# Performance work log

Hardware: AMD Instinct MI355X
Metric: run time of the kernel (lower is better)

## Reference

```python
import jax, jax.numpy as jnp
import numpy as np

DT = 0.1
EM_DX_DUMMY = 100.0  # dummy_value_set['em_delta_x']
EM_DV_DUMMY = 0.0    # dummy_value_set['em_delta_v']
ALPHA = 0.3          # keras LeakyReLU default
B, T, F = 32768, 50, 11
PROJ, U = 64, 128
MC = 3
IN_DIM = PROJ + U + 6 + MC  # 201


def setup_inputs() -> dict:
    key = jax.random.key(0)
    ks = jax.random.split(key, 16)
    def rn(k, shape, scale=0.05):
        return jax.random.normal(k, shape, dtype=jnp.float32) * scale
    return {
        'proj_latent': rn(ks[0], (B, PROJ), 1.0),
        'enc_h': rn(ks[1], (B, U), 1.0),
        'idm_s': jax.random.uniform(ks[2], (B, T, F), dtype=jnp.float32),
        'merger_cs': rn(ks[3], (B, T, MC), 1.0),
        'scaler_mean': rn(ks[4], (6,), 1.0),
        'scaler_var': jax.random.uniform(ks[5], (6,), dtype=jnp.float32) + 0.5,
        'W_lstm': rn(ks[6], (IN_DIM, 4 * U)),
        'U_lstm': rn(ks[7], (U, 4 * U)),
        'b_lstm': jnp.zeros((4 * U,), jnp.float32),
        'W1': rn(ks[8], (U, U)), 'b1': jnp.zeros((U,), jnp.float32),
        'W2': rn(ks[9], (U, U)), 'b2': jnp.zeros((U,), jnp.float32),
        'W3': rn(ks[10], (U, U)), 'b3': jnp.zeros((U,), jnp.float32),
        'Wa': rn(ks[11], (U, 1)), 'ba': jnp.zeros((1,), jnp.float32),
    }


def _lrelu(v):
    return jnp.where(v > 0, v, ALPHA * v)


def reference(proj_latent, enc_h, idm_s, merger_cs, scaler_mean, scaler_var,
              W_lstm, U_lstm, b_lstm, W1, b1, W2, b2, W3, b3, Wa, ba):
    b = idm_s.shape[0]
    u = W1.shape[0]
    inv_std = 1.0 / jnp.sqrt(scaler_var)

    def step(carry, xs):
        h, c, ego_v, ego_x, disp, prev_act = carry
        s, mc, t = xs  # s: [b,F], mc: [b,MC]
        first = (t == 0)
        f_veh_v = s[:, 1:2]
        m_veh_v = s[:, 2:3]
        f_glob_x = s[:, 4:5]
        m_glob_x = s[:, 5:6]
        m_exists = s[:, -1:]
        # physics update (skipped at step 0 where state is read from idm_s)
        new_v = jnp.where(first, s[:, 0:1], ego_v + prev_act * DT)
        delta = new_v * DT + 0.5 * prev_act * DT * DT
        new_x = jnp.where(first, s[:, 3:4], ego_x + delta)
        new_d = jnp.where(first, jnp.zeros_like(disp), disp + delta)
        ef_dx = f_glob_x - new_x
        em_dx = (m_glob_x - new_x) * m_exists + (1.0 - m_exists) * EM_DX_DUMMY
        ef_dv = new_v - f_veh_v
        em_dv = (new_v - m_veh_v) * m_exists + (1.0 - m_exists) * EM_DV_DUMMY
        env = jnp.concatenate([new_v, f_veh_v, ef_dv, ef_dx, em_dv, em_dx], axis=-1)
        env = (env - scaler_mean) * inv_std
        inp = jnp.concatenate([proj_latent, enc_h, env, mc], axis=-1)  # [b, 201]
        # keras LSTM cell: gate order i, f, g(candidate), o
        z = inp @ W_lstm + h @ U_lstm + b_lstm
        i = jax.nn.sigmoid(z[:, :u])
        f = jax.nn.sigmoid(z[:, u:2 * u])
        g = jnp.tanh(z[:, 2 * u:3 * u])
        o = jax.nn.sigmoid(z[:, 3 * u:])
        c2 = f * c + i * g
        h2 = o * jnp.tanh(c2)
        x1 = _lrelu(h2 @ W1 + b1)
        x2 = _lrelu(x1 @ W2 + b2)
        x3 = _lrelu(x2 @ W3 + b3)
        act = x3 @ Wa + ba  # [b, 1]
        return (h2, c2, new_v, new_x, new_d, act), (new_d, act)

    z1 = jnp.zeros((b, u), jnp.float32)
    one = jnp.zeros((b, 1), jnp.float32)
    carry0 = (z1, z1, one, one, one, one)
    xs = (jnp.swapaxes(idm_s, 0, 1), jnp.swapaxes(merger_cs, 0, 1),
          jnp.arange(idm_s.shape[1]))
    _, (disp_seq, act_seq) = jax.lax.scan(step, carry0, xs)
    # [T,b,1] -> [b,T,1]
    return jnp.swapaxes(disp_seq, 0, 1), jnp.swapaxes(act_seq, 0, 1)
```

## Files before the change

kernel.cpp:

```cpp
#include <hip/hip_runtime.h>

typedef unsigned short ushort_t;
typedef unsigned int uint_t;
typedef __bf16 v8bf __attribute__((ext_vector_type(8)));
typedef float v4f __attribute__((ext_vector_type(4)));

#define DTC 0.1f
#define NB 32768
#define NT 50

union U8 { v8bf v; ushort_t s[8]; };

__device__ __forceinline__ ushort_t f2bf(float f) {
  uint_t u = __float_as_uint(f);
  u += 0x7fffu + ((u >> 16) & 1u);
  return (ushort_t)(u >> 16);
}
__device__ __forceinline__ float bf2f(ushort_t s) {
  return __uint_as_float(((uint_t)s) << 16);
}
__device__ __forceinline__ float sigm(float x) {
  return __builtin_amdgcn_rcpf(1.f + __expf(-x));
}
__device__ __forceinline__ float tanhf_(float x) {
  return 1.f - 2.f * __builtin_amdgcn_rcpf(1.f + __expf(2.f * x));
}

__device__ __forceinline__ v8bf opaque(v8bf x) {
  union { v8bf v; uint_t u[4]; } t; t.v = x;
  asm volatile("" : "+v"(t.u[0]), "+v"(t.u[1]), "+v"(t.u[2]), "+v"(t.u[3]));
  return t.v;
}


__global__ __launch_bounds__(512) __attribute__((amdgpu_waves_per_eu(2, 2)))
void fsim_kernel(
    const float* __restrict__ proj, const float* __restrict__ ench,
    const float* __restrict__ idm,  const float* __restrict__ mcs,
    const float* __restrict__ smean,const float* __restrict__ svar,
    const float* __restrict__ Wl,   const float* __restrict__ Ul,
    const float* __restrict__ bl,   const float* __restrict__ W1,
    const float* __restrict__ b1,   const float* __restrict__ W2,
    const float* __restrict__ b2,   const float* __restrict__ W3,
    const float* __restrict__ b3,   const float* __restrict__ Wa,
    const float* __restrict__ ba,   float* __restrict__ out) {
  __shared__ __align__(16) short sh[81184];
  short* pe   = sh;
  short* hA   = sh;
  short* hB   = sh + 8704;
  short* xa_s = sh + 17408;
  short* ex_s = sh + 26112;
  float* sdf  = (float*)(sh + 28672);
  float* carr = (float*)(sh + 31232);
  float* wa_s = (float*)(sh + 31744);
  float* nrm  = (float*)(sh + 32000);
  short* u_lds= sh + 32032;

  const int tid  = threadIdx.x;
  const int wg   = blockIdx.x;
  const int w    = tid >> 6;
  const int l    = tid & 63;
  const int quad = l >> 4;
  const int c16  = l & 15;
  const int colz = w * 16 + c16;

  float* out_disp = out;
  float* out_act  = out + (size_t)NB * NT;

  const int eA = tid / 10, fA = tid - eA * 10;
  const float* pfpA; int pstA;
  if (fA < 7) { pfpA = idm + (size_t)(wg * 64 + eA) * 550 + ((fA == 6) ? 10 : fA); pstA = 11; }
  else        { pfpA = mcs + (size_t)(wg * 64 + eA) * 150 + (fA - 7);              pstA = 3;  }
  const int iB = tid + 512;
  const int eB = iB / 10, fB = iB - eB * 10;
  const float* pfpB; int pstB;
  if (fB < 7) { pfpB = idm + (size_t)(wg * 64 + eB) * 550 + ((fB == 6) ? 10 : fB); pstB = 11; }
  else        { pfpB = mcs + (size_t)(wg * 64 + eB) * 150 + (fB - 7);              pstB = 3;  }
  float pfA = pfpA[0];
  float pfB = (tid < 128) ? pfpB[0] : 0.f;

#pragma unroll
  for (int kc = 0; kc < 3; ++kc) {
#pragma unroll
    for (int g = 0; g < 4; ++g) {
      U8 u;
#pragma unroll
      for (int j = 0; j < 8; ++j)
        u.s[j] = f2bf(Ul[(kc * 32 + quad * 8 + j) * 512 + g * 128 + colz]);
      *(v8bf*)(u_lds + ((kc * 4 + g) * 512 + tid) * 8) = u.v;
    }
  }
  v8bf Uf3[4];
#pragma unroll
  for (int g = 0; g < 4; ++g) {
    U8 u;
#pragma unroll
    for (int j = 0; j < 8; ++j)
      u.s[j] = f2bf(Ul[(96 + quad * 8 + j) * 512 + g * 128 + colz]);
    Uf3[g] = opaque(u.v);
  }
  v8bf Ef[4];
#pragma unroll
  for (int g = 0; g < 4; ++g) {
    U8 u;
#pragma unroll
    for (int j = 0; j < 8; ++j) {
      int kk = quad * 8 + j;
      ushort_t val = 0;
      if (kk < 27) {
        int jj = kk % 9;
        float wv = Wl[(192 + jj) * 512 + g * 128 + colz];
        ushort_t hi = f2bf(wv);
        val = (kk < 9) ? hi : ((kk < 18) ? f2bf(wv - bf2f(hi)) : hi);
      }
      u.s[j] = val;
    }
    Ef[g] = opaque(u.v);
  }
  v8bf W1f[4], W2f[4], W3f[4];
#pragma unroll
  for (int kc = 0; kc < 4; ++kc) {
    U8 a, b, c;
#pragma unroll
    for (int j = 0; j < 8; ++j) {
      int row = kc * 32 + quad * 8 + j;
      a.s[j] = f2bf(W1[row * 128 + colz]);
      b.s[j] = f2bf(W2[row * 128 + colz]);
      c.s[j] = f2bf(W3[row * 128 + colz]);
    }
    W1f[kc] = opaque(a.v); W2f[kc] = opaque(b.v); W3f[kc] = opaque(c.v);
  }
  float bias1 = b1[colz], bias2 = b2[colz], bias3 = b3[colz];
  float ba_v  = ba[0];

  for (int i = tid; i < 2560; i += 512) ex_s[i] = 0;
  if (tid < 6) { nrm[tid] = smean[tid]; nrm[6 + tid] = 1.f / sqrtf(svar[tid]); }
  if (tid < 128) wa_s[tid] = Wa[tid];
  sdf[tid] = pfA;
  if (tid < 128) sdf[512 + tid] = pfB;

  for (int i = tid; i < 64 * 192; i += 512) {
    int e = i / 192, j = i - e * 192;
    float v = (j < 64) ? proj[(wg * 64 + e) * 64 + j]
                       : ench[(wg * 64 + e) * 128 + (j - 64)];
    pe[e * 200 + j] = (short)f2bf(v);
  }
  __syncthreads();

  uint_t base_pk[4][8];
#pragma unroll
  for (int mt = 0; mt < 4; ++mt) {
    v4f accz[4];
#pragma unroll
    for (int g = 0; g < 4; ++g) {
      float bz = bl[g * 128 + colz];
      accz[g] = (v4f){bz, bz, bz, bz};
    }
    for (int kc = 0; kc < 6; ++kc) {
      const v8bf a = *(const v8bf*)(pe + (mt * 16 + c16) * 200 + kc * 32 + quad * 8);
#pragma unroll
      for (int g = 0; g < 4; ++g) {
        U8 bu;
#pragma unroll
        for (int j = 0; j < 8; ++j)
          bu.s[j] = f2bf(Wl[(kc * 32 + quad * 8 + j) * 512 + g * 128 + colz]);
        accz[g] = __builtin_amdgcn_mfma_f32_16x16x32_bf16(a, bu.v, accz[g], 0, 0, 0);
      }
    }
#pragma unroll
    for (int g = 0; g < 4; ++g) {
      base_pk[mt][g * 2 + 0] = (uint_t)f2bf(accz[g][0]) | ((uint_t)f2bf(accz[g][1]) << 16);
      base_pk[mt][g * 2 + 1] = (uint_t)f2bf(accz[g][2]) | ((uint_t)f2bf(accz[g][3]) << 16);
    }
  }
  __syncthreads();

  for (int i = tid; i < 8704; i += 512) hA[i] = 0;

  v4f c_st[4];
#pragma unroll
  for (int mt = 0; mt < 4; ++mt) c_st[mt] = (v4f){0.f, 0.f, 0.f, 0.f};

  for (int t = 0; t < NT; ++t) {
    short* rd = (t & 1) ? hB : hA;
    short* wr = (t & 1) ? hA : hB;

    if (t + 1 < NT) {
      pfA = pfpA[(size_t)(t + 1) * pstA];
      if (tid < 128) pfB = pfpB[(size_t)(t + 1) * pstB];
    }

    if ((l & 7) == 0) {
      const int e  = w * 8 + (l >> 3);
      const int ge = wg * 64 + e;
      const float* sp = sdf + (t & 1) * 640 + e * 10;
      float s0 = sp[0], s1 = sp[1], s2 = sp[2], s3 = sp[3];
      float s4 = sp[4], s5 = sp[5], s10 = sp[6];
      float mc0 = sp[7], mc1 = sp[8], mc2 = sp[9];
      float pa = 0.f, vv = 0.f, xx = 0.f, dd = 0.f;
      if (t != 0) { pa = carr[192 + e]; vv = carr[e]; xx = carr[64 + e]; dd = carr[128 + e]; }
      float new_v = (t == 0) ? s0 : vv + pa * DTC;
      float delta = new_v * DTC + 0.5f * pa * DTC * DTC;
      float new_x = (t == 0) ? s3 : xx + delta;
      float new_d = (t == 0) ? 0.f : dd + delta;
      float env[9];
      env[0] = new_v;
      env[1] = s1;
      env[2] = new_v - s1;
      env[3] = s4 - new_x;
      env[4] = (new_v - s2) * s10;
      env[5] = (s5 - new_x) * s10 + (1.f - s10) * 100.f;
#pragma unroll
      for (int j = 0; j < 6; ++j) env[j] = (env[j] - nrm[j]) * nrm[6 + j];
      env[6] = mc0; env[7] = mc1; env[8] = mc2;
#pragma unroll
      for (int j = 0; j < 9; ++j) {
        ushort_t hi = f2bf(env[j]);
        ushort_t lo = f2bf(env[j] - bf2f(hi));
        ex_s[e * 40 + j]      = (short)hi;
        ex_s[e * 40 + 9 + j]  = (short)hi;
        ex_s[e * 40 + 18 + j] = (short)lo;
      }
      carr[e] = new_v; carr[64 + e] = new_x; carr[128 + e] = new_d;
      out_disp[(size_t)ge * NT + t] = new_d;
    }
    __syncthreads();

#pragma unroll
    for (int half = 0; half < 2; ++half) {
      v4f acc[2][4];
#pragma unroll
      for (int m2 = 0; m2 < 2; ++m2) {
        int mt = half * 2 + m2;
#pragma unroll
        for (int g = 0; g < 4; ++g) {
          uint_t w0 = base_pk[mt][g * 2 + 0], w1 = base_pk[mt][g * 2 + 1];
          acc[m2][g][0] = __uint_as_float(w0 << 16);
          acc[m2][g][1] = __uint_as_float(w0 & 0xffff0000u);
          acc[m2][g][2] = __uint_as_float(w1 << 16);
          acc[m2][g][3] = __uint_as_float(w1 & 0xffff0000u);
        }
      }
      {
        const v8bf ax0 = *(const v8bf*)(ex_s + ((half * 2 + 0) * 16 + c16) * 40 + quad * 8);
        const v8bf ax1 = *(const v8bf*)(ex_s + ((half * 2 + 1) * 16 + c16) * 40 + quad * 8);
#pragma unroll
        for (int g = 0; g < 4; ++g) {
          acc[0][g] = __builtin_amdgcn_mfma_f32_16x16x32_bf16(ax0, Ef[g], acc[0][g], 0, 0, 0);
          acc[1][g] = __builtin_amdgcn_mfma_f32_16x16x32_bf16(ax1, Ef[g], acc[1][g], 0, 0, 0);
        }
      }
#pragma unroll
      for (int kc = 0; kc < 4; ++kc) {
        const v8bf a0 = *(const v8bf*)(rd + ((half * 2 + 0) * 16 + c16) * 136 + kc * 32 + quad * 8);
        const v8bf a1 = *(const v8bf*)(rd + ((half * 2 + 1) * 16 + c16) * 136 + kc * 32 + quad * 8);
#pragma unroll
        for (int g = 0; g < 4; ++g) {
          v8bf uf;
          if (kc < 3) uf = *(const v8bf*)(u_lds + ((kc * 4 + g) * 512 + tid) * 8);
          else        uf = Uf3[g];
          acc[0][g] = __builtin_amdgcn_mfma_f32_16x16x32_bf16(a0, uf, acc[0][g], 0, 0, 0);
          acc[1][g] = __builtin_amdgcn_mfma_f32_16x16x32_bf16(a1, uf, acc[1][g], 0, 0, 0);
        }
      }
#pragma unroll
      for (int m2 = 0; m2 < 2; ++m2) {
        int mt = half * 2 + m2;
        v4f cc = c_st[mt], h2;
#pragma unroll
        for (int r = 0; r < 4; ++r) {
          float ig = sigm(acc[m2][0][r]);
          float fg = sigm(acc[m2][1][r]);
          float gg = tanhf_(acc[m2][2][r]);
          float og = sigm(acc[m2][3][r]);
          float c2 = fg * cc[r] + ig * gg;
          cc[r] = c2;
          h2[r] = og * tanhf_(c2);
        }
        c_st[mt] = cc;
#pragma unroll
        for (int r = 0; r < 4; ++r)
          wr[(mt * 16 + quad * 4 + r) * 136 + colz] = (short)f2bf(h2[r]);
      }
    }
    __syncthreads();

    auto mlp_layer = [&](const short* S, const v8bf* Wf, float bias, short* D) {
      v4f xs[4];
#pragma unroll
      for (int mt = 0; mt < 4; ++mt) {
        v4f acc = (v4f){bias, bias, bias, bias};
#pragma unroll
        for (int kc = 0; kc < 4; ++kc) {
          const v8bf a = *(const v8bf*)(S + (mt * 16 + c16) * 136 + kc * 32 + quad * 8);
          acc = __builtin_amdgcn_mfma_f32_16x16x32_bf16(a, Wf[kc], acc, 0, 0, 0);
        }
#pragma unroll
        for (int r = 0; r < 4; ++r) { float v = acc[r]; acc[r] = (v > 0.f) ? v : 0.3f * v; }
        xs[mt] = acc;
      }
#pragma unroll
      for (int mt = 0; mt < 4; ++mt)
#pragma unroll
        for (int r = 0; r < 4; ++r)
          D[(mt * 16 + quad * 4 + r) * 136 + colz] = (short)f2bf(xs[mt][r]);
    };
    mlp_layer(wr,   W1f, bias1, xa_s);
    __syncthreads();
    mlp_layer(xa_s, W2f, bias2, rd);
    __syncthreads();
    mlp_layer(rd,   W3f, bias3, xa_s);
    if (t + 1 < NT) {
      sdf[((t + 1) & 1) * 640 + tid] = pfA;
      if (tid < 128) sdf[((t + 1) & 1) * 640 + 512 + tid] = pfB;
    }
    __syncthreads();

    {
      const int r = w * 8 + (l >> 3);
      const int p = l & 7;
      float s = 0.f;
#pragma unroll
      for (int i = 0; i < 16; ++i) {
        int u = p * 16 + i;
        s += bf2f((ushort_t)xa_s[r * 136 + u]) * wa_s[u];
      }
      s += __shfl_xor(s, 1);
      s += __shfl_xor(s, 2);
      s += __shfl_xor(s, 4);
      if ((l & 7) == 0) {
        float a = s + ba_v;
        carr[192 + r] = a;
        out_act[(size_t)(wg * 64 + r) * NT + t] = a;
      }
    }
  }
}

extern "C" void kernel_launch(void* const* d_in, const int* in_sizes, int n_in,
                              void* d_out, int out_size, void* d_ws, size_t ws_size,
                              hipStream_t stream) {
  (void)in_sizes; (void)n_in; (void)out_size; (void)d_ws; (void)ws_size;
  fsim_kernel<<<dim3(512), dim3(512), 0, stream>>>(
      (const float*)d_in[0],  (const float*)d_in[1],  (const float*)d_in[2],
      (const float*)d_in[3],  (const float*)d_in[4],  (const float*)d_in[5],
      (const float*)d_in[6],  (const float*)d_in[7],  (const float*)d_in[8],
      (const float*)d_in[9],  (const float*)d_in[10], (const float*)d_in[11],
      (const float*)d_in[12], (const float*)d_in[13], (const float*)d_in[14],
      (const float*)d_in[15], (const float*)d_in[16], (float*)d_out);
}
```

Before: 1.017 ms.

## Keep all LSTM recurrent and MLP weight fragments resident in AGPRs instead of LDS

Moves the bf16 U_lstm fragments, which were partly staged in LDS, into register arrays, and pins all persistent weight fragments (U, E, W1-3) to accumulator registers (AGPRs) through an inline-asm constraint. This removes the per-step LDS reads of recurrent weights and shrinks shared memory from about 162KB to about 64KB. The output-head dot product now uses two 16-byte vector LDS loads instead of sixteen scalar loads. The risk is register pressure: the AGPR budget at 2 waves/EU could overflow, and the compiler may insert copies from AGPR to VGPR before each MFMA.

Result: slower. 1.799 ms (+76.8%).

```diff
diff --git a/kernel.cpp b/kernel.cpp
--- a/kernel.cpp
+++ b/kernel.cpp
@@ -26,9 +26,9 @@
   return 1.f - 2.f * __builtin_amdgcn_rcpf(1.f + __expf(2.f * x));
 }
 
-__device__ __forceinline__ v8bf opaque(v8bf x) {
+__device__ __forceinline__ v8bf opaque_a(v8bf x) {
   union { v8bf v; uint_t u[4]; } t; t.v = x;
-  asm volatile("" : "+v"(t.u[0]), "+v"(t.u[1]), "+v"(t.u[2]), "+v"(t.u[3]));
+  asm volatile("" : "+a"(t.u[0]), "+a"(t.u[1]), "+a"(t.u[2]), "+a"(t.u[3]));
   return t.v;
 }
 
@@ -44,7 +44,7 @@
     const float* __restrict__ b2,   const float* __restrict__ W3,
     const float* __restrict__ b3,   const float* __restrict__ Wa,
     const float* __restrict__ ba,   float* __restrict__ out) {
-  __shared__ __align__(16) short sh[81184];
+  __shared__ __align__(16) short sh[32032];
   short* pe   = sh;
   short* hA   = sh;
   short* hB   = sh + 8704;
@@ -54,7 +54,6 @@
   float* carr = (float*)(sh + 31232);
   float* wa_s = (float*)(sh + 31744);
   float* nrm  = (float*)(sh + 32000);
-  short* u_lds= sh + 32032;
 
   const int tid  = threadIdx.x;
   const int wg   = blockIdx.x;
@@ -79,25 +78,17 @@
   float pfA = pfpA[0];
   float pfB = (tid < 128) ? pfpB[0] : 0.f;
 
-#pragma unroll
-  for (int kc = 0; kc < 3; ++kc) {
+  v8bf Uf[4][4];
+#pragma unroll
+  for (int kc = 0; kc < 4; ++kc) {
 #pragma unroll
     for (int g = 0; g < 4; ++g) {
       U8 u;
 #pragma unroll
       for (int j = 0; j < 8; ++j)
         u.s[j] = f2bf(Ul[(kc * 32 + quad * 8 + j) * 512 + g * 128 + colz]);
-      *(v8bf*)(u_lds + ((kc * 4 + g) * 512 + tid) * 8) = u.v;
-    }
-  }
-  v8bf Uf3[4];
-#pragma unroll
-  for (int g = 0; g < 4; ++g) {
-    U8 u;
-#pragma unroll
-    for (int j = 0; j < 8; ++j)
-      u.s[j] = f2bf(Ul[(96 + quad * 8 + j) * 512 + g * 128 + colz]);
-    Uf3[g] = opaque(u.v);
+      Uf[kc][g] = opaque_a(u.v);
+    }
   }
   v8bf Ef[4];
 #pragma unroll
@@ -115,7 +106,7 @@
       }
       u.s[j] = val;
     }
-    Ef[g] = opaque(u.v);
+    Ef[g] = opaque_a(u.v);
   }
   v8bf W1f[4], W2f[4], W3f[4];
 #pragma unroll
@@ -128,7 +119,7 @@
       b.s[j] = f2bf(W2[row * 128 + colz]);
       c.s[j] = f2bf(W3[row * 128 + colz]);
     }
-    W1f[kc] = opaque(a.v); W2f[kc] = opaque(b.v); W3f[kc] = opaque(c.v);
+    W1f[kc] = opaque_a(a.v); W2f[kc] = opaque_a(b.v); W3f[kc] = opaque_a(c.v);
   }
   float bias1 = b1[colz], bias2 = b2[colz], bias3 = b3[colz];
   float ba_v  = ba[0];
@@ -256,11 +247,8 @@
         const v8bf a1 = *(const v8bf*)(rd + ((half * 2 + 1) * 16 + c16) * 136 + kc * 32 + quad * 8);
 #pragma unroll
         for (int g = 0; g < 4; ++g) {
-          v8bf uf;
-          if (kc < 3) uf = *(const v8bf*)(u_lds + ((kc * 4 + g) * 512 + tid) * 8);
-          else        uf = Uf3[g];
-          acc[0][g] = __builtin_amdgcn_mfma_f32_16x16x32_bf16(a0, uf, acc[0][g], 0, 0, 0);
-          acc[1][g] = __builtin_amdgcn_mfma_f32_16x16x32_bf16(a1, uf, acc[1][g], 0, 0, 0);
+          acc[0][g] = __builtin_amdgcn_mfma_f32_16x16x32_bf16(a0, Uf[kc][g], acc[0][g], 0, 0, 0);
+          acc[1][g] = __builtin_amdgcn_mfma_f32_16x16x32_bf16(a1, Uf[kc][g], acc[1][g], 0, 0, 0);
         }
       }
 #pragma unroll
@@ -319,12 +307,14 @@
     {
       const int r = w * 8 + (l >> 3);
       const int p = l & 7;
+      U8 va, vb;
+      va.v = *(const v8bf*)(xa_s + r * 136 + p * 16);
+      vb.v = *(const v8bf*)(xa_s + r * 136 + p * 16 + 8);
       float s = 0.f;
 #pragma unroll
-      for (int i = 0; i < 16; ++i) {
-        int u = p * 16 + i;
-        s += bf2f((ushort_t)xa_s[r * 136 + u]) * wa_s[u];
-      }
+      for (int i = 0; i < 8; ++i) s += bf2f(va.s[i]) * wa_s[p * 16 + i];
+#pragma unroll
+      for (int i = 0; i < 8; ++i) s += bf2f(vb.s[i]) * wa_s[p * 16 + 8 + i];
       s += __shfl_xor(s, 1);
       s += __shfl_xor(s, 2);
       s += __shfl_xor(s, 4);
```
